# Performance work log

Hardware: AMD Instinct MI355X
Metric: run time of the kernel (lower is better)

## Reference

```python
import jax, jax.numpy as jnp
import numpy as np

B, IN_DIM, OUT_DIM = 4096, 4096, 4096

def setup_inputs() -> dict:
    key = jax.random.key(0)
    kx, kw, kb = jax.random.split(key, 3)
    x = jax.random.normal(kx, (B, IN_DIM), dtype=jnp.float32)
    W = jax.random.normal(kw, (OUT_DIM, IN_DIM), dtype=jnp.float32) * (1.0 / np.sqrt(IN_DIM))
    b = jax.random.normal(kb, (OUT_DIM,), dtype=jnp.float32) * (1.0 / np.sqrt(IN_DIM))
    return {"x": x, "W": W, "b": b}

def reference(x, W, b):
    # Original computes sum over in_dim of x[:, :, None] * W.T[None, :, :],
    # which is exactly x @ W.T. NOTE: bias is added TWICE in the source
    # (duplicated `out += self.b`), so the faithful output is x @ W.T + 2*b.
    out = jnp.einsum('bi,oi->bo', x, W)  # [B, out_dim]
    out = out + 2.0 * b
    return out
```

## Files before the change

kernel.cpp:

```cpp
#include <hip/hip_runtime.h>
#include <hip/hip_bf16.h>
#include <utility>


typedef short bf16x8 __attribute__((ext_vector_type(8)));
typedef short s16x4  __attribute__((ext_vector_type(4)));
typedef short s16x8  __attribute__((ext_vector_type(8)));
typedef float f32x4  __attribute__((ext_vector_type(4)));

constexpr int MDIM = 4096, NDIM = 4096, KDIM = 4096;

typedef const __attribute__((address_space(1))) void* gas_t;
typedef __attribute__((address_space(3))) void*       las_t;

__device__ __forceinline__ short f2bf(float f) {
    __hip_bfloat16 h = __float2bfloat16(f);
    short s; __builtin_memcpy(&s, &h, 2); return s;
}

__global__ __launch_bounds__(256)
void cvt2_f32_bf16(const float* __restrict__ inA, const float* __restrict__ inB,
                   short* __restrict__ outA, short* __restrict__ outB, int n8each) {
    int idx    = blockIdx.x * blockDim.x + threadIdx.x;
    int stride = gridDim.x * blockDim.x;
    for (int i = idx; i < 2 * n8each; i += stride) {
        const f32x4* in4 = (i < n8each) ? (const f32x4*)inA : (const f32x4*)inB;
        s16x8*      out8 = (i < n8each) ? (s16x8*)outA      : (s16x8*)outB;
        int j = (i < n8each) ? i : i - n8each;
        f32x4 a = in4[2 * j];
        f32x4 b = in4[2 * j + 1];
        s16x8 o = { f2bf(a[0]), f2bf(a[1]), f2bf(a[2]), f2bf(a[3]),
                    f2bf(b[0]), f2bf(b[1]), f2bf(b[2]), f2bf(b[3]) };
        out8[j] = o;
    }
}

constexpr int BM = 256, BN = 256, BK = 64;
constexpr int NT  = KDIM / BK;
constexpr int ASZ = BM * BK;
constexpr int BSZ = BN * BK;

template <int Q, bool LGKM8, class StageFn>
__device__ __forceinline__ void phase(const short* Ab, int rA, int c0, int c1,
                                      bf16x8 (&bf)[4][2], f32x4 (&acc)[8][4],
                                      StageFn&& stage) {
    bf16x8 af[2][2];
    #pragma unroll
    for (int m = 0; m < 2; ++m) {
        const short* p = &Ab[(rA + Q * 32 + m * 16) * BK];
        af[m][0] = *(const bf16x8*)(p + c0);
        af[m][1] = *(const bf16x8*)(p + c1);
    }
    stage();
    if (LGKM8) asm volatile("s_waitcnt lgkmcnt(8)" ::: "memory");
    __builtin_amdgcn_s_barrier();
    __builtin_amdgcn_s_setprio(1);
    #pragma unroll
    for (int m = 0; m < 2; ++m)
        #pragma unroll
        for (int ni = 0; ni < 4; ++ni)
            #pragma unroll
            for (int kk = 0; kk < 2; ++kk)
                acc[Q * 2 + m][ni] = __builtin_amdgcn_mfma_f32_16x16x32_bf16(
                    af[m][kk], bf[ni][kk], acc[Q * 2 + m][ni], 0, 0, 0);
    __builtin_amdgcn_s_setprio(0);
}

__global__ __launch_bounds__(512, 2)
void gemm_bf16_256(const short* __restrict__ Xb, const short* __restrict__ Wb,
                   const float* __restrict__ Bv, float* __restrict__ Out)
{
    __shared__ short lds[2 * ASZ + 2 * BSZ];

    const int tid  = threadIdx.x;
    const int lane = tid & 63;
    const int wid  = tid >> 6;
    const int wr   = wid >> 2;
    const int wc   = wid & 3;

    const int bid = blockIdx.x;
    const int lin = (bid & 7) * 32 + (bid >> 3);
    const int tm0 = (lin >> 4) * BM;
    const int tn0 = (lin & 15) * BN;

    const int srow = lane >> 3;
    const int sgrn = (lane & 7) ^ srow;
    const char* xbase = (const char*)Xb;
    const char* wbase = (const char*)Wb;
    int aOff[2][2], bOff[2][2], dOff[2][2];
    #pragma unroll
    for (int h = 0; h < 2; ++h) {
        #pragma unroll
        for (int j = 0; j < 2; ++j) {
            const int r = h * 128 + (2 * wid + j) * 8;
            aOff[h][j] = ((tm0 + r + srow) * KDIM + sgrn * 8) * 2;
            bOff[h][j] = ((tn0 + r + srow) * KDIM + sgrn * 8) * 2;
            dOff[h][j] = r * BK;
        }
    }

    const int g   = lane >> 4;
    const int r16 = lane & 15;
    const int c0  = ((0 + g) ^ (r16 & 7)) * 8;
    const int c1  = ((4 + g) ^ (r16 & 7)) * 8;
    const int rA  = wr * 128 + r16;
    const int rB  = wc * 64  + r16;

    f32x4 acc[8][4] = {};

    auto tile_body = [&](auto par_ic, int t) {
        constexpr int PAR = decltype(par_ic)::value;
        const short* Ab = (const short*)&lds[PAR * ASZ];
        const short* Bb = (const short*)&lds[2 * ASZ + PAR * BSZ];
        short* dstA = (short*)&lds[(PAR ^ 1) * ASZ];
        short* dstB = (short*)&lds[2 * ASZ + PAR * BSZ];

        auto stageA = [&](int kt, int h) {
            const size_t kb = (size_t)kt * (BK * 2);
            __builtin_amdgcn_global_load_lds((gas_t)(xbase + kb + aOff[h][0]),
                                             (las_t)(dstA + dOff[h][0]), 16, 0, 0);
            __builtin_amdgcn_global_load_lds((gas_t)(xbase + kb + aOff[h][1]),
                                             (las_t)(dstA + dOff[h][1]), 16, 0, 0);
        };
        auto stageB = [&](int kt, int h) {
            const size_t kb = (size_t)kt * (BK * 2);
            __builtin_amdgcn_global_load_lds((gas_t)(wbase + kb + bOff[h][0]),
                                             (las_t)(dstB + dOff[h][0]), 16, 0, 0);
            __builtin_amdgcn_global_load_lds((gas_t)(wbase + kb + bOff[h][1]),
                                             (las_t)(dstB + dOff[h][1]), 16, 0, 0);
        };

        bf16x8 bf[4][2];
        #pragma unroll
        for (int ni = 0; ni < 4; ++ni) {
            const short* p = &Bb[(rB + ni * 16) * BK];
            bf[ni][0] = *(const bf16x8*)(p + c0);
            bf[ni][1] = *(const bf16x8*)(p + c1);
        }
        phase<0, true>(Ab, rA, c0, c1, bf, acc,
                       [&] { if (t + 1 < NT) { stageA(t + 1, 0); stageA(t + 1, 1); } });
        __builtin_amdgcn_s_barrier();
        phase<1, false>(Ab, rA, c0, c1, bf, acc,
                        [&] { if (t + 2 < NT) stageB(t + 2, 0); });
        __builtin_amdgcn_s_barrier();
        phase<2, false>(Ab, rA, c0, c1, bf, acc,
                        [&] { if (t + 2 < NT) stageB(t + 2, 1); });
        __builtin_amdgcn_s_barrier();
        phase<3, false>(Ab, rA, c0, c1, bf, acc, [&] {});
        if (t < NT - 2)       { asm volatile("s_waitcnt vmcnt(4)" ::: "memory"); }
        else if (t == NT - 2) { asm volatile("s_waitcnt vmcnt(0)" ::: "memory"); }
        __builtin_amdgcn_s_barrier();
    };

    {
        short* dA0 = (short*)&lds[0];
        short* dB0 = (short*)&lds[2 * ASZ];
        short* dB1 = (short*)&lds[2 * ASZ + BSZ];
        #pragma unroll
        for (int h = 0; h < 2; ++h) {
            __builtin_amdgcn_global_load_lds((gas_t)(wbase + bOff[h][0]), (las_t)(dB0 + dOff[h][0]), 16, 0, 0);
            __builtin_amdgcn_global_load_lds((gas_t)(wbase + bOff[h][1]), (las_t)(dB0 + dOff[h][1]), 16, 0, 0);
        }
        #pragma unroll
        for (int h = 0; h < 2; ++h) {
            __builtin_amdgcn_global_load_lds((gas_t)(xbase + aOff[h][0]), (las_t)(dA0 + dOff[h][0]), 16, 0, 0);
            __builtin_amdgcn_global_load_lds((gas_t)(xbase + aOff[h][1]), (las_t)(dA0 + dOff[h][1]), 16, 0, 0);
        }
        #pragma unroll
        for (int h = 0; h < 2; ++h) {
            __builtin_amdgcn_global_load_lds((gas_t)(wbase + (BK * 2) + bOff[h][0]), (las_t)(dB1 + dOff[h][0]), 16, 0, 0);
            __builtin_amdgcn_global_load_lds((gas_t)(wbase + (BK * 2) + bOff[h][1]), (las_t)(dB1 + dOff[h][1]), 16, 0, 0);
        }
        asm volatile("s_waitcnt vmcnt(4)" ::: "memory");
        __builtin_amdgcn_s_barrier();
    }

    for (int t = 0; t < NT; t += 2) {
        tile_body(std::integral_constant<int, 0>{}, t);
        tile_body(std::integral_constant<int, 1>{}, t + 1);
    }

    float bb[4];
    #pragma unroll
    for (int ni = 0; ni < 4; ++ni)
        bb[ni] = 2.0f * Bv[tn0 + wc * 64 + ni * 16 + r16];

    #pragma unroll
    for (int mi = 0; mi < 8; ++mi) {
        #pragma unroll
        for (int r = 0; r < 4; ++r) {
            const int row = tm0 + wr * 128 + mi * 16 + g * 4 + r;
            float* orow = Out + (size_t)row * NDIM + tn0 + wc * 64 + r16;
            #pragma unroll
            for (int ni = 0; ni < 4; ++ni)
                orow[ni * 16] = acc[mi][ni][r] + bb[ni];
        }
    }
}

constexpr int FBM = 128, FBN = 128, FBK = 32, LDT = FBK + 8;
__global__ __launch_bounds__(256)
void gemm_xwt_bias2(const float* __restrict__ X, const float* __restrict__ W,
                    const float* __restrict__ Bv, float* __restrict__ Out)
{
    __shared__ short As[FBM * LDT];
    __shared__ short Bs[FBN * LDT];
    const int tid  = threadIdx.x;
    const int lane = tid & 63;
    const int wid  = tid >> 6;
    const int wr   = wid >> 1;
    const int wc   = wid & 1;
    const int tm0  = blockIdx.y * FBM;
    const int tn0  = blockIdx.x * FBN;
    const int srow = tid >> 3;
    const int scol = (tid & 7) * 4;
    const int g    = lane >> 4;
    const int r16  = lane & 15;
    f32x4 acc[4][4] = {};
    const float* xg = X + (size_t)(tm0 + srow) * KDIM + scol;
    const float* wg = W + (size_t)(tn0 + srow) * KDIM + scol;
    for (int k0 = 0; k0 < KDIM; k0 += FBK) {
        #pragma unroll
        for (int i = 0; i < 4; ++i) {
            const int row = srow + 32 * i;
            f32x4 av = *(const f32x4*)(xg + (size_t)(32 * i) * KDIM + k0);
            f32x4 bv = *(const f32x4*)(wg + (size_t)(32 * i) * KDIM + k0);
            s16x4 pa = { f2bf(av[0]), f2bf(av[1]), f2bf(av[2]), f2bf(av[3]) };
            s16x4 pb = { f2bf(bv[0]), f2bf(bv[1]), f2bf(bv[2]), f2bf(bv[3]) };
            *(s16x4*)&As[row * LDT + scol] = pa;
            *(s16x4*)&Bs[row * LDT + scol] = pb;
        }
        __syncthreads();
        bf16x8 af[4], bfr[4];
        #pragma unroll
        for (int mi = 0; mi < 4; ++mi)
            af[mi] = *(const bf16x8*)&As[(wr * 64 + mi * 16 + r16) * LDT + g * 8];
        #pragma unroll
        for (int ni = 0; ni < 4; ++ni)
            bfr[ni] = *(const bf16x8*)&Bs[(wc * 64 + ni * 16 + r16) * LDT + g * 8];
        #pragma unroll
        for (int mi = 0; mi < 4; ++mi)
            #pragma unroll
            for (int ni = 0; ni < 4; ++ni)
                acc[mi][ni] = __builtin_amdgcn_mfma_f32_16x16x32_bf16(
                                  af[mi], bfr[ni], acc[mi][ni], 0, 0, 0);
        __syncthreads();
    }
    float bb[4];
    #pragma unroll
    for (int ni = 0; ni < 4; ++ni)
        bb[ni] = 2.0f * Bv[tn0 + wc * 64 + ni * 16 + r16];
    #pragma unroll
    for (int mi = 0; mi < 4; ++mi)
        #pragma unroll
        for (int r = 0; r < 4; ++r) {
            const int row = tm0 + wr * 64 + mi * 16 + g * 4 + r;
            float* orow = Out + (size_t)row * NDIM + tn0 + wc * 64 + r16;
            #pragma unroll
            for (int ni = 0; ni < 4; ++ni)
                orow[ni * 16] = acc[mi][ni][r] + bb[ni];
        }
}

extern "C" void kernel_launch(void* const* d_in, const int* in_sizes, int n_in,
                              void* d_out, int out_size, void* d_ws, size_t ws_size,
                              hipStream_t stream) {
    const float* X  = (const float*)d_in[0];
    const float* W  = (const float*)d_in[1];
    const float* Bv = (const float*)d_in[2];
    float* Out = (float*)d_out;

    const size_t nElem = (size_t)MDIM * KDIM;
    const size_t need  = 2 * nElem * sizeof(short);

    if (ws_size >= need) {
        short* Xb = (short*)d_ws;
        short* Wb = Xb + nElem;
        const int n8 = (int)(nElem / 8);
        cvt2_f32_bf16<<<4096, 256, 0, stream>>>(X, W, Xb, Wb, n8);
        gemm_bf16_256<<<dim3(256), 512, 0, stream>>>(Xb, Wb, Bv, Out);
    } else {
        dim3 grid(NDIM / FBN, MDIM / FBM);
        gemm_xwt_bias2<<<grid, 256, 0, stream>>>(X, W, Bv, Out);
    }
}
```

Before: 140.9 us.

## Software-pipeline LDS fragment reads across tiles and cut per-phase barriers

Restructures the GEMM main loop so each phase's A-fragment LDS reads are issued one phase ahead of the MFMAs that consume them. The B fragments and first A quarter for the next K tile are prefetched into ping-pong register sets during the current tile. The four per-phase barriers per tile are reduced to two. The aim is to hide LDS read latency behind MFMA work and remove synchronization stalls, at the cost of more live VGPRs (double-buffered B/A0 fragments) and tighter reasoning about LDS buffer hazards.

New measurement: 386.6 us. +174.4%, slower.

```diff
diff --git a/kernel.cpp b/kernel.cpp
--- a/kernel.cpp
+++ b/kernel.cpp
@@ -40,20 +40,20 @@
 constexpr int ASZ = BM * BK;
 constexpr int BSZ = BN * BK;
 
-template <int Q, bool LGKM8, class StageFn>
-__device__ __forceinline__ void phase(const short* Ab, int rA, int c0, int c1,
-                                      bf16x8 (&bf)[4][2], f32x4 (&acc)[8][4],
-                                      StageFn&& stage) {
-    bf16x8 af[2][2];
+template <int Q>
+__device__ __forceinline__ void read_aq(const short* base, int rA, int c0, int c1,
+                                        bf16x8 (&dst)[2][2]) {
     #pragma unroll
     for (int m = 0; m < 2; ++m) {
-        const short* p = &Ab[(rA + Q * 32 + m * 16) * BK];
-        af[m][0] = *(const bf16x8*)(p + c0);
-        af[m][1] = *(const bf16x8*)(p + c1);
-    }
-    stage();
-    if (LGKM8) asm volatile("s_waitcnt lgkmcnt(8)" ::: "memory");
-    __builtin_amdgcn_s_barrier();
+        const short* p = &base[(rA + Q * 32 + m * 16) * BK];
+        dst[m][0] = *(const bf16x8*)(p + c0);
+        dst[m][1] = *(const bf16x8*)(p + c1);
+    }
+}
+
+template <int Q>
+__device__ __forceinline__ void mfma_quad(const bf16x8 (&af)[2][2], const bf16x8 (&bf)[4][2],
+                                          f32x4 (&acc)[8][4]) {
     __builtin_amdgcn_s_setprio(1);
     #pragma unroll
     for (int m = 0; m < 2; ++m)
@@ -108,10 +108,16 @@
 
     f32x4 acc[8][4] = {};
 
-    auto tile_body = [&](auto par_ic, int t) {
+    bf16x8 bSetA[4][2], bSetB[4][2];
+    bf16x8 a0SetA[2][2], a0SetB[2][2];
+
+    auto tile_body = [&](auto par_ic, int t,
+                         const bf16x8 (&bcur)[4][2], bf16x8 (&bnxt)[4][2],
+                         const bf16x8 (&a0cur)[2][2], bf16x8 (&a0nxt)[2][2]) {
         constexpr int PAR = decltype(par_ic)::value;
-        const short* Ab = (const short*)&lds[PAR * ASZ];
-        const short* Bb = (const short*)&lds[2 * ASZ + PAR * BSZ];
+        const short* Ab  = (const short*)&lds[PAR * ASZ];
+        const short* AbN = (const short*)&lds[(PAR ^ 1) * ASZ];
+        const short* BbN = (const short*)&lds[2 * ASZ + (PAR ^ 1) * BSZ];
         short* dstA = (short*)&lds[(PAR ^ 1) * ASZ];
         short* dstB = (short*)&lds[2 * ASZ + PAR * BSZ];
 
@@ -130,26 +136,35 @@
                                              (las_t)(dstB + dOff[h][1]), 16, 0, 0);
         };
 
-        bf16x8 bf[4][2];
-        #pragma unroll
-        for (int ni = 0; ni < 4; ++ni) {
-            const short* p = &Bb[(rB + ni * 16) * BK];
-            bf[ni][0] = *(const bf16x8*)(p + c0);
-            bf[ni][1] = *(const bf16x8*)(p + c1);
-        }
-        phase<0, true>(Ab, rA, c0, c1, bf, acc,
-                       [&] { if (t + 1 < NT) { stageA(t + 1, 0); stageA(t + 1, 1); } });
-        __builtin_amdgcn_s_barrier();
-        phase<1, false>(Ab, rA, c0, c1, bf, acc,
-                        [&] { if (t + 2 < NT) stageB(t + 2, 0); });
-        __builtin_amdgcn_s_barrier();
-        phase<2, false>(Ab, rA, c0, c1, bf, acc,
-                        [&] { if (t + 2 < NT) stageB(t + 2, 1); });
-        __builtin_amdgcn_s_barrier();
-        phase<3, false>(Ab, rA, c0, c1, bf, acc, [&] {});
-        if (t < NT - 2)       { asm volatile("s_waitcnt vmcnt(4)" ::: "memory"); }
-        else if (t == NT - 2) { asm volatile("s_waitcnt vmcnt(0)" ::: "memory"); }
-        __builtin_amdgcn_s_barrier();
+        bf16x8 aq1[2][2];
+        read_aq<1>(Ab, rA, c0, c1, aq1);
+        if (t + 1 < NT) { stageA(t + 1, 0); stageA(t + 1, 1); }
+        mfma_quad<0>(a0cur, bcur, acc);
+
+        bf16x8 aq2[2][2];
+        read_aq<2>(Ab, rA, c0, c1, aq2);
+        if (t + 2 < NT) stageB(t + 2, 0);
+        mfma_quad<1>(aq1, bcur, acc);
+
+        bf16x8 aq3[2][2];
+        read_aq<3>(Ab, rA, c0, c1, aq3);
+        if (t + 2 < NT) stageB(t + 2, 1);
+        if (t < NT - 2) { asm volatile("s_waitcnt vmcnt(4)" ::: "memory"); }
+        else            { asm volatile("s_waitcnt vmcnt(0)" ::: "memory"); }
+        asm volatile("s_barrier" ::: "memory");
+        mfma_quad<2>(aq2, bcur, acc);
+
+        if (t + 1 < NT) {
+            #pragma unroll
+            for (int ni = 0; ni < 4; ++ni) {
+                const short* p = &BbN[(rB + ni * 16) * BK];
+                bnxt[ni][0] = *(const bf16x8*)(p + c0);
+                bnxt[ni][1] = *(const bf16x8*)(p + c1);
+            }
+            read_aq<0>(AbN, rA, c0, c1, a0nxt);
+        }
+        mfma_quad<3>(aq3, bcur, acc);
+        asm volatile("s_barrier" ::: "memory");
     };
 
     {
@@ -172,12 +187,20 @@
             __builtin_amdgcn_global_load_lds((gas_t)(wbase + (BK * 2) + bOff[h][1]), (las_t)(dB1 + dOff[h][1]), 16, 0, 0);
         }
         asm volatile("s_waitcnt vmcnt(4)" ::: "memory");
-        __builtin_amdgcn_s_barrier();
+        asm volatile("s_barrier" ::: "memory");
+        const short* Bb0 = (const short*)&lds[2 * ASZ];
+        #pragma unroll
+        for (int ni = 0; ni < 4; ++ni) {
+            const short* p = &Bb0[(rB + ni * 16) * BK];
+            bSetA[ni][0] = *(const bf16x8*)(p + c0);
+            bSetA[ni][1] = *(const bf16x8*)(p + c1);
+        }
+        read_aq<0>((const short*)&lds[0], rA, c0, c1, a0SetA);
     }
 
     for (int t = 0; t < NT; t += 2) {
-        tile_body(std::integral_constant<int, 0>{}, t);
-        tile_body(std::integral_constant<int, 1>{}, t + 1);
+        tile_body(std::integral_constant<int, 0>{}, t,     bSetA, bSetB, a0SetA, a0SetB);
+        tile_body(std::integral_constant<int, 1>{}, t + 1, bSetB, bSetA, a0SetB, a0SetA);
     }
 
     float bb[4];
```
